# Performance work log

Hardware: AMD Instinct MI355X
Metric: run time of the kernel (lower is better)

Reference implementation:

```python
import jax, jax.numpy as jnp
import numpy as np

B, S, D, H = 4, 2048, 1024, 16
DK = D // H


def setup_inputs() -> dict:
    key = jax.random.key(0)
    ks = jax.random.split(key, 12)
    s = 1.0 / np.sqrt(D)
    inp = {
        "q": jax.random.normal(ks[0], (B, S, D), jnp.float32),
        "k": jax.random.normal(ks[1], (B, S, D), jnp.float32),
        "v": jax.random.normal(ks[2], (B, S, D), jnp.float32),
        # causal mask, broadcastable over batch and heads
        "mask": jnp.tril(jnp.ones((S, S), jnp.int32))[None, None, :, :],
        "Wq": jax.random.uniform(ks[3], (D, D), jnp.float32, -s, s),
        "bq": jax.random.uniform(ks[4], (D,), jnp.float32, -s, s),
        "Wk": jax.random.uniform(ks[5], (D, D), jnp.float32, -s, s),
        "bk": jax.random.uniform(ks[6], (D,), jnp.float32, -s, s),
        "Wv": jax.random.uniform(ks[7], (D, D), jnp.float32, -s, s),
        "bv": jax.random.uniform(ks[8], (D,), jnp.float32, -s, s),
        "Wo": jax.random.uniform(ks[9], (D, D), jnp.float32, -s, s),
        "bo": jax.random.uniform(ks[10], (D,), jnp.float32, -s, s),
    }
    return inp


def reference(q, k, v, mask, Wq, bq, Wk, bk, Wv, bv, Wo, bo):
    def split_heads(x):  # [B,S,D] -> [B,H,S,DK]
        return x.reshape(B, S, H, DK).transpose(0, 2, 1, 3)

    qh = split_heads(q @ Wq.T + bq)
    kh = split_heads(k @ Wk.T + bk)
    vh = split_heads(v @ Wv.T + bv)

    scores = jnp.einsum("bhqd,bhkd->bhqk", qh, kh) / jnp.sqrt(jnp.float32(DK))
    scores = jnp.where(mask == 0, jnp.float32(-1e9), scores)
    attn = jax.nn.softmax(scores, axis=-1)
    out = jnp.einsum("bhqk,bhkd->bhqd", attn, vh)
    out = out.transpose(0, 2, 1, 3).reshape(B, S, D)
    return out @ Wo.T + bo
```

## Files before the change

### kernel.cpp

```cpp
#include <hip/hip_runtime.h>
#include <cstdint>

#define Bb 4
#define Ss 2048
#define Dd 1024
#define Hh 16

typedef unsigned short u16;
typedef unsigned int u32;
typedef __attribute__((ext_vector_type(8))) short short8;
typedef __attribute__((ext_vector_type(8))) _Float16 half8;
typedef __attribute__((ext_vector_type(2))) __fp16 fp16x2;
typedef __attribute__((ext_vector_type(4))) float floatx4;
typedef __attribute__((ext_vector_type(16))) float floatx16;
typedef __attribute__((address_space(3))) u32 lds_u32;
typedef const __attribute__((address_space(1))) u32 glob_u32;

__device__ __forceinline__ u16 f2bf(float x) {
  union { float f; u32 u; } v; v.f = x;
  u32 r = v.u + 0x7fffu + ((v.u >> 16) & 1u);
  return (u16)(r >> 16);
}

__device__ __forceinline__ u32 pk2(float a, float b) {
  union { fp16x2 h; u32 u; } cv;
  cv.h = __builtin_amdgcn_cvt_pkrtz(a, b);
  return cv.u;
}

__device__ __forceinline__ half8 h8_from(u32 a, u32 b, u32 c, u32 d) {
  union { u32 u[4]; half8 h; } t;
  t.u[0] = a; t.u[1] = b; t.u[2] = c; t.u[3] = d;
  return t.h;
}

__global__ __launch_bounds__(256) void cvt_many(const float* __restrict__ s0,
                                                const float* __restrict__ s1,
                                                const float* __restrict__ s2,
                                                const float* __restrict__ s3,
                                                u16* __restrict__ d0,
                                                u16* __restrict__ d1,
                                                u16* __restrict__ d2,
                                                u16* __restrict__ d3, int n8) {
  int z = blockIdx.y;
  const float* s = z == 0 ? s0 : z == 1 ? s1 : z == 2 ? s2 : s3;
  u16* d = z == 0 ? d0 : z == 1 ? d1 : z == 2 ? d2 : d3;
  int i = blockIdx.x * 256 + threadIdx.x;
  if (i >= n8) return;
  const float4* sp = (const float4*)s;
  float4 a = sp[2 * i], b = sp[2 * i + 1];
  u32 w0 = (u32)f2bf(a.x) | ((u32)f2bf(a.y) << 16);
  u32 w1 = (u32)f2bf(a.z) | ((u32)f2bf(a.w) << 16);
  u32 w2 = (u32)f2bf(b.x) | ((u32)f2bf(b.y) << 16);
  u32 w3 = (u32)f2bf(b.z) | ((u32)f2bf(b.w) << 16);
  ((uint4*)d)[i] = make_uint4(w0, w1, w2, w3);
}

template <int MODE>
__device__ __forceinline__ void gemm_body(const u16* __restrict__ A,
                                          const u16* __restrict__ Bw,
                                          const float* __restrict__ bias,
                                          void* __restrict__ Cout, float scale) {
  __shared__ u16 As[128 * 64];
  __shared__ u16 Bs[128 * 64];
  int tid = threadIdx.x;
  int wave = tid >> 6, lane = tid & 63;
  int quad = lane >> 4, l16 = lane & 15;
  int m0 = blockIdx.x * 128, n0 = blockIdx.y * 128;
  int wr = (wave >> 1) * 64, wc = (wave & 1) * 64;
  int s7 = l16 & 7;
  int srow = wave * 8 + (lane >> 3);
  int gcol = (((lane & 7) ^ (lane >> 3)) << 3);

  floatx4 vzero = {0.f, 0.f, 0.f, 0.f};
  floatx4 acc[4][4];
#pragma unroll
  for (int i = 0; i < 4; ++i)
#pragma unroll
    for (int j = 0; j < 4; ++j) acc[i][j] = vzero;

  for (int kt = 0; kt < Dd; kt += 64) {
    __syncthreads();
#pragma unroll
    for (int c = 0; c < 4; ++c) {
      int r = c * 32 + srow;
      __builtin_amdgcn_global_load_lds(
          (glob_u32*)&A[(size_t)(m0 + r) * Dd + kt + gcol],
          (lds_u32*)&As[(c * 32 + wave * 8) * 64], 16, 0, 0);
      __builtin_amdgcn_global_load_lds(
          (glob_u32*)&Bw[(size_t)(n0 + r) * Dd + kt + gcol],
          (lds_u32*)&Bs[(c * 32 + wave * 8) * 64], 16, 0, 0);
    }
    __syncthreads();
#pragma unroll
    for (int kk = 0; kk < 2; ++kk) {
      short8 af[4], bf[4];
#pragma unroll
      for (int i = 0; i < 4; ++i)
        af[i] = *(const short8*)&As[(wr + i * 16 + l16) * 64 + (((quad + 4 * kk) ^ s7) << 3)];
#pragma unroll
      for (int j = 0; j < 4; ++j)
        bf[j] = *(const short8*)&Bs[(wc + j * 16 + l16) * 64 + (((quad + 4 * kk) ^ s7) << 3)];
#pragma unroll
      for (int i = 0; i < 4; ++i)
#pragma unroll
        for (int j = 0; j < 4; ++j)
          acc[i][j] = __builtin_amdgcn_mfma_f32_16x16x32_bf16(af[i], bf[j], acc[i][j], 0, 0, 0);
    }
  }

#pragma unroll
  for (int i = 0; i < 4; ++i) {
#pragma unroll
    for (int j = 0; j < 4; ++j) {
#pragma unroll
      for (int r = 0; r < 4; ++r) {
        int m = m0 + wr + i * 16 + quad * 4 + r;
        int n = n0 + wc + j * 16 + l16;
        float val = (acc[i][j][r] + bias[n]) * scale;
        if (MODE == 0) {
          int b = m >> 11, s = m & (Ss - 1);
          int h = n >> 6, dk = n & 63;
          ((u16*)Cout)[((((size_t)b * Hh + h) * Ss + s) << 6) + dk] = f2bf(val);
        } else {
          ((float*)Cout)[(size_t)m * Dd + n] = val;
        }
      }
    }
  }
}

__global__ __launch_bounds__(256) void gemm_qkv(const u16* qb, const u16* kb, const u16* vb,
                                                const u16* Wq, const u16* Wk, const u16* Wv,
                                                const float* bq, const float* bk, const float* bv,
                                                u16* qo, u16* ko, u16* vo) {
  const float K1 = 0.18033688f;
  int z = blockIdx.z;
  const u16* A = z == 0 ? qb : z == 1 ? kb : vb;
  const u16* W = z == 0 ? Wq : z == 1 ? Wk : Wv;
  const float* bi = z == 0 ? bq : z == 1 ? bk : bv;
  u16* o = z == 0 ? qo : z == 1 ? ko : vo;
  gemm_body<0>(A, W, bi, o, z == 0 ? K1 : 1.0f);
}

__global__ __launch_bounds__(256) void gemm_out(const u16* A, const u16* W,
                                                const float* bi, float* o) {
  gemm_body<1>(A, W, bi, o, 1.0f);
}

__global__ __launch_bounds__(256) void transpose_v(const u16* __restrict__ in,
                                                   _Float16* __restrict__ out) {
  __shared__ u16 T[64 * 72];
  int bh = blockIdx.y, s0 = blockIdx.x * 64, tid = threadIdx.x;
#pragma unroll
  for (int c = 0; c < 2; ++c) {
    int e = c * 2048 + tid * 8;
    int r = e >> 6, col = e & 63;
    *(uint4*)&T[r * 72 + col] = *(const uint4*)&in[((size_t)bh * Ss + s0 + r) * 64 + col];
  }
  __syncthreads();
#pragma unroll
  for (int c = 0; c < 2; ++c) {
    int e = c * 2048 + tid * 8;
    int d = e >> 6, sc = e & 63;
    _Float16 tmp[8];
#pragma unroll
    for (int j = 0; j < 8; ++j) {
      union { u32 u; float f; } cv;
      cv.u = (u32)T[(sc + j) * 72 + d] << 16;
      tmp[j] = (_Float16)cv.f;
    }
    *(uint4*)&out[((size_t)bh * 64 + d) * Ss + s0 + sc] = *(uint4*)tmp;
  }
}

#define MFIX 4.0f
#define SW(a, b) asm("v_permlane32_swap_b32 %0, %1" : "+v"(a), "+v"(b))
#define VRD(CH, NT) \
  (*(const half8*)&Vt[p][((NT) * 32 + l31) * 64 + ((((CH) + hi) ^ s7b) << 3)])

#define TILE_BODY(NST, MASKED)                                                \
  do {                                                                        \
    short8 kf0[4], kf1[4];                                                    \
    _Pragma("unroll") for (int m = 0; m < 4; ++m) {                           \
      kf0[m] = *(const short8*)&Kt[p][l31 * 64 + (((2 * m + hi) ^ s7b) << 3)];\
      if (NST == 2)                                                           \
        kf1[m] = *(const short8*)&Kt[p][(32 + l31) * 64 +                     \
                                        (((2 * m + hi) ^ s7b) << 3)];         \
    }                                                                         \
    floatx16 sc0, sc1;                                                        \
    _Pragma("unroll") for (int r = 0; r < 16; ++r) {                          \
      sc0[r] = -MFIX;                                                         \
      sc1[r] = -MFIX;                                                         \
    }                                                                         \
    __builtin_amdgcn_s_setprio(1);                                            \
    _Pragma("unroll") for (int m = 0; m < 4; ++m) {                           \
      sc0 = __builtin_amdgcn_mfma_f32_32x32x16_bf16(kf0[m], qf[m], sc0, 0, 0, 0); \
      if (NST == 2)                                                           \
        sc1 = __builtin_amdgcn_mfma_f32_32x32x16_bf16(kf1[m], qf[m], sc1, 0, 0, 0); \
    }                                                                         \
    __builtin_amdgcn_s_setprio(0);                                            \
    if (MASKED) {                                                             \
      int qrow = Rq + l31;                                                    \
      _Pragma("unroll") for (int r = 0; r < 16; ++r) {                        \
        int key = k0 + 4 * hi + (r & 3) + 8 * (r >> 2);                       \
        if (key > qrow) sc0[r] = -3e38f;                                      \
        if (NST == 2 && key + 32 > qrow) sc1[r] = -3e38f;                     \
      }                                                                       \
    }                                                                         \
    u32 c0[8], c1[8];                                                         \
    float rs = 0.f;                                                           \
    _Pragma("unroll") for (int j = 0; j < 8; ++j) {                           \
      float p0 = __builtin_amdgcn_exp2f(sc0[2 * j]);                          \
      float p1 = __builtin_amdgcn_exp2f(sc0[2 * j + 1]);                      \
      rs += p0 + p1;                                                          \
      c0[j] = pk2(p0, p1);                                                    \
      if (NST == 2) {                                                         \
        float p2 = __builtin_amdgcn_exp2f(sc1[2 * j]);                        \
        float p3 = __builtin_amdgcn_exp2f(sc1[2 * j + 1]);                    \
        rs += p2 + p3;                                                        \
        c1[j] = pk2(p2, p3);                                                  \
      }                                                                       \
    }                                                                         \
    l_part += rs;                                                             \
    SW(c0[0], c0[2]); SW(c0[1], c0[3]); SW(c0[4], c0[6]); SW(c0[5], c0[7]);   \
    if (NST == 2) {                                                           \
      SW(c1[0], c1[2]); SW(c1[1], c1[3]); SW(c1[4], c1[6]); SW(c1[5], c1[7]); \
    }                                                                         \
    __builtin_amdgcn_s_setprio(1);                                            \
    {                                                                         \
      half8 pa = h8_from(c0[0], c0[1], c0[2], c0[3]);                         \
      o0 = __builtin_amdgcn_mfma_f32_32x32x16_f16(pa, VRD(0, 0), o0, 0, 0, 0);\
      o1 = __builtin_amdgcn_mfma_f32_32x32x16_f16(pa, VRD(0, 1), o1, 0, 0, 0);\
      half8 pb = h8_from(c0[4], c0[5], c0[6], c0[7]);                         \
      o0 = __builtin_amdgcn_mfma_f32_32x32x16_f16(pb, VRD(2, 0), o0, 0, 0, 0);\
      o1 = __builtin_amdgcn_mfma_f32_32x32x16_f16(pb, VRD(2, 1), o1, 0, 0, 0);\
      if (NST == 2) {                                                         \
        half8 pc = h8_from(c1[0], c1[1], c1[2], c1[3]);                       \
        o0 = __builtin_amdgcn_mfma_f32_32x32x16_f16(pc, VRD(4, 0), o0, 0, 0, 0); \
        o1 = __builtin_amdgcn_mfma_f32_32x32x16_f16(pc, VRD(4, 1), o1, 0, 0, 0); \
        half8 pd = h8_from(c1[4], c1[5], c1[6], c1[7]);                       \
        o0 = __builtin_amdgcn_mfma_f32_32x32x16_f16(pd, VRD(6, 0), o0, 0, 0, 0); \
        o1 = __builtin_amdgcn_mfma_f32_32x32x16_f16(pd, VRD(6, 1), o1, 0, 0, 0); \
      }                                                                       \
    }                                                                         \
    __builtin_amdgcn_s_setprio(0);                                            \
  } while (0)

__global__ __launch_bounds__(256) void attn_kernel(const u16* __restrict__ qh,
                                                   const u16* __restrict__ kh,
                                                   const _Float16* __restrict__ vT,
                                                   u16* __restrict__ ctx) {
  __shared__ u16 Kt[2][64 * 64];
  __shared__ _Float16 Vt[2][64 * 64];

  int tid = threadIdx.x, w = tid >> 6, lane = tid & 63;
  int hi = lane >> 5, l31 = lane & 31, s7b = lane & 7;
  int bh = blockIdx.x;
  int sp = blockIdx.y;
  const u16* Q = qh + (size_t)bh * Ss * 64;
  const u16* K = kh + (size_t)bh * Ss * 64;
  const _Float16* V = vT + (size_t)bh * 64 * Ss;

  int Rq = (w < 2) ? 64 * sp + 32 * w : 64 * (31 - sp) + 32 * (w - 2);

  short8 qf[4];
#pragma unroll
  for (int m = 0; m < 4; ++m)
    qf[m] = *(const short8*)&Q[(size_t)(Rq + l31) * 64 + m * 16 + hi * 8];

  floatx16 o0, o1;
#pragma unroll
  for (int r = 0; r < 16; ++r) { o0[r] = 0.f; o1[r] = 0.f; }
  float l_part = 0.f;

  int lrow = w * 8 + (lane >> 3);
  int g8 = ((lane & 7) ^ (lane >> 3)) << 3;
  int nkt = 32 - sp;

#define STAGE(P, KT)                                                          \
  do {                                                                        \
    int _k0 = (KT) * 64;                                                      \
    __builtin_amdgcn_global_load_lds(                                         \
        (glob_u32*)&K[(size_t)(_k0 + lrow) * 64 + g8],                        \
        (lds_u32*)&Kt[P][w * 512], 16, 0, 0);                                 \
    __builtin_amdgcn_global_load_lds(                                         \
        (glob_u32*)&K[(size_t)(_k0 + 32 + lrow) * 64 + g8],                   \
        (lds_u32*)&Kt[P][2048 + w * 512], 16, 0, 0);                          \
    __builtin_amdgcn_global_load_lds(                                         \
        (glob_u32*)&V[(size_t)lrow * Ss + _k0 + g8],                          \
        (lds_u32*)&Vt[P][w * 512], 16, 0, 0);                                 \
    __builtin_amdgcn_global_load_lds(                                         \
        (glob_u32*)&V[(size_t)(32 + lrow) * Ss + _k0 + g8],                   \
        (lds_u32*)&Vt[P][2048 + w * 512], 16, 0, 0);                          \
  } while (0)

  STAGE(0, 0);

  int p = 0;
  for (int kt = 0; kt < nkt; ++kt) {
    int k0 = kt * 64;
    __syncthreads();
    if (kt + 1 < nkt) STAGE(p ^ 1, kt + 1);

    if (k0 + 63 <= Rq) {
      TILE_BODY(2, false);
    } else if (k0 <= Rq + 31) {
      if (k0 + 32 <= Rq + 31) TILE_BODY(2, true);
      else TILE_BODY(1, true);
    }
    p ^= 1;
  }
#undef STAGE

  float l2 = l_part + __shfl_xor(l_part, 32, 64);
  float linv = 1.0f / l2;
  int b = bh >> 4, h = bh & 15;
#pragma unroll
  for (int r = 0; r < 16; ++r) {
    int qi = (r & 3) + 8 * (r >> 2) + 4 * hi;
    float li = __shfl(linv, qi, 64);
    size_t base = ((size_t)b * Ss + Rq + qi) * Dd + h * 64 + l31;
    ctx[base] = f2bf(o0[r] * li);
    ctx[base + 32] = f2bf(o1[r] * li);
  }
}

extern "C" void kernel_launch(void* const* d_in, const int* in_sizes, int n_in,
                              void* d_out, int out_size, void* d_ws, size_t ws_size,
                              hipStream_t stream) {
  const float* q = (const float*)d_in[0];
  const float* k = (const float*)d_in[1];
  const float* v = (const float*)d_in[2];
  const float* Wq = (const float*)d_in[4];
  const float* bq = (const float*)d_in[5];
  const float* Wk = (const float*)d_in[6];
  const float* bk = (const float*)d_in[7];
  const float* Wv = (const float*)d_in[8];
  const float* bv = (const float*)d_in[9];
  const float* Wo = (const float*)d_in[10];
  const float* bo = (const float*)d_in[11];

  char* ws = (char*)d_ws;
  const size_t MB = 1024 * 1024;
  u16* qb = (u16*)(ws + 0 * MB);
  u16* kb = (u16*)(ws + 16 * MB);
  u16* vb = (u16*)(ws + 32 * MB);
  u16* Wqb = (u16*)(ws + 48 * MB);
  u16* Wkb = (u16*)(ws + 50 * MB);
  u16* Wvb = (u16*)(ws + 52 * MB);
  u16* Wob = (u16*)(ws + 54 * MB);
  u16* qhp = (u16*)(ws + 56 * MB);
  u16* khp = (u16*)(ws + 72 * MB);
  u16* vhp = (u16*)(ws + 88 * MB);
  _Float16* vhT = (_Float16*)kb;
  u16* ctx = qb;

  const int nQKV8 = (Bb * Ss * Dd) / 8;
  const int nW8 = (Dd * Dd) / 8;
  {
    dim3 g(nQKV8 / 256, 3);
    cvt_many<<<g, 256, 0, stream>>>(q, k, v, v, qb, kb, vb, vb, nQKV8);
  }
  {
    dim3 g(nW8 / 256, 4);
    cvt_many<<<g, 256, 0, stream>>>(Wq, Wk, Wv, Wo, Wqb, Wkb, Wvb, Wob, nW8);
  }
  {
    dim3 g((Bb * Ss) / 128, Dd / 128, 3);
    gemm_qkv<<<g, 256, 0, stream>>>(qb, kb, vb, Wqb, Wkb, Wvb, bq, bk, bv, qhp, khp, vhp);
  }
  {
    dim3 g(Ss / 64, Bb * Hh);
    transpose_v<<<g, 256, 0, stream>>>(vhp, vhT);
  }
  {
    dim3 g(Bb * Hh, 16);
    attn_kernel<<<g, 256, 0, stream>>>(qhp, khp, vhT, ctx);
  }
  {
    dim3 g((Bb * Ss) / 128, Dd / 128);
    gemm_out<<<g, 256, 0, stream>>>(ctx, Wob, bo, (float*)d_out);
  }
}
```

Measured before the change: 335.3 us.

## Rewrite projection GEMMs as 256x128 double-buffered pipelined kernel with 8 waves

```diff
diff --git a/kernel.cpp b/kernel.cpp
--- a/kernel.cpp
+++ b/kernel.cpp
@@ -56,21 +56,45 @@
   ((uint4*)d)[i] = make_uint4(w0, w1, w2, w3);
 }
 
+#define MFMA_B16 __builtin_amdgcn_mfma_f32_16x16x32_bf16
+
 template <int MODE>
-__device__ __forceinline__ void gemm_body(const u16* __restrict__ A,
-                                          const u16* __restrict__ Bw,
-                                          const float* __restrict__ bias,
-                                          void* __restrict__ Cout, float scale) {
-  __shared__ u16 As[128 * 64];
-  __shared__ u16 Bs[128 * 64];
+__device__ __forceinline__ void gemm256_body(const u16* __restrict__ A,
+                                             const u16* __restrict__ Bw,
+                                             const float* __restrict__ bias,
+                                             void* __restrict__ Cout, float scale) {
+  __shared__ u16 Sa[2][2][128 * 64];
+  __shared__ u16 Sb[2][2][64 * 64];
   int tid = threadIdx.x;
-  int wave = tid >> 6, lane = tid & 63;
+  int w = tid >> 6, lane = tid & 63;
+  int wm = w >> 1, wn = w & 1;
   int quad = lane >> 4, l16 = lane & 15;
-  int m0 = blockIdx.x * 128, n0 = blockIdx.y * 128;
-  int wr = (wave >> 1) * 64, wc = (wave & 1) * 64;
-  int s7 = l16 & 7;
-  int srow = wave * 8 + (lane >> 3);
-  int gcol = (((lane & 7) ^ (lane >> 3)) << 3);
+  int s7 = l16 & 15 & 7;
+  int m0 = blockIdx.x * 256, n0 = blockIdx.y * 128;
+  int srow = tid >> 3;
+  int gcol = (((tid & 7) ^ ((tid >> 3) & 7)) << 3);
+  int ha = wm >> 1;
+  int ra = (wm & 1) * 64;
+
+#define SG_A(BUF, KT)                                                         \
+  do {                                                                        \
+    _Pragma("unroll") for (int h = 0; h < 2; ++h)                             \
+    _Pragma("unroll") for (int j = 0; j < 2; ++j)                             \
+      __builtin_amdgcn_global_load_lds(                                       \
+          (glob_u32*)&A[(size_t)(m0 + h * 128 + j * 64 + srow) * Dd +         \
+                        (KT) * 64 + gcol],                                    \
+          (lds_u32*)&Sa[BUF][h][(j * 64 + w * 8) * 64], 16, 0, 0);            \
+  } while (0)
+#define SG_B(BUF, G, KT)                                                      \
+  __builtin_amdgcn_global_load_lds(                                           \
+      (glob_u32*)&Bw[(size_t)(n0 + (G) * 64 + srow) * Dd + (KT) * 64 + gcol], \
+      (lds_u32*)&Sb[BUF][G][(w * 8) * 64], 16, 0, 0)
+#define LDA(BUF, I, KK)                                                       \
+  (*(const short8*)&Sa[BUF][ha][(ra + (I) * 16 + l16) * 64 +                  \
+                                ((((KK) * 4 + quad) ^ s7) << 3)])
+#define LDB(BUF, G, J, KK)                                                    \
+  (*(const short8*)&Sb[BUF][G][(wn * 32 + (J) * 16 + l16) * 64 +              \
+                               ((((KK) * 4 + quad) ^ s7) << 3)])
 
   floatx4 vzero = {0.f, 0.f, 0.f, 0.f};
   floatx4 acc[4][4];
@@ -79,45 +103,97 @@
 #pragma unroll
     for (int j = 0; j < 4; ++j) acc[i][j] = vzero;
 
-  for (int kt = 0; kt < Dd; kt += 64) {
-    __syncthreads();
-#pragma unroll
-    for (int c = 0; c < 4; ++c) {
-      int r = c * 32 + srow;
-      __builtin_amdgcn_global_load_lds(
-          (glob_u32*)&A[(size_t)(m0 + r) * Dd + kt + gcol],
-          (lds_u32*)&As[(c * 32 + wave * 8) * 64], 16, 0, 0);
-      __builtin_amdgcn_global_load_lds(
-          (glob_u32*)&Bw[(size_t)(n0 + r) * Dd + kt + gcol],
-          (lds_u32*)&Bs[(c * 32 + wave * 8) * 64], 16, 0, 0);
-    }
-    __syncthreads();
-#pragma unroll
-    for (int kk = 0; kk < 2; ++kk) {
-      short8 af[4], bf[4];
-#pragma unroll
-      for (int i = 0; i < 4; ++i)
-        af[i] = *(const short8*)&As[(wr + i * 16 + l16) * 64 + (((quad + 4 * kk) ^ s7) << 3)];
-#pragma unroll
-      for (int j = 0; j < 4; ++j)
-        bf[j] = *(const short8*)&Bs[(wc + j * 16 + l16) * 64 + (((quad + 4 * kk) ^ s7) << 3)];
-#pragma unroll
-      for (int i = 0; i < 4; ++i)
-#pragma unroll
-        for (int j = 0; j < 4; ++j)
-          acc[i][j] = __builtin_amdgcn_mfma_f32_16x16x32_bf16(af[i], bf[j], acc[i][j], 0, 0, 0);
-    }
-  }
+  SG_A(0, 0);
+  SG_B(0, 0, 0);
+  SG_B(0, 1, 0);
+  asm volatile("s_waitcnt vmcnt(0)" ::: "memory");
+  __builtin_amdgcn_s_barrier();
+  __builtin_amdgcn_sched_barrier(0);
+
+  const int nkt = Dd / 64;
+  for (int kt = 0; kt < nkt; ++kt) {
+    int bu = kt & 1, nb = bu ^ 1;
+    int pre = (kt + 1 < nkt);
+    int kn = kt + 1;
+
+    short8 a00 = LDA(bu, 0, 0), a01 = LDA(bu, 0, 1);
+    short8 a10 = LDA(bu, 1, 0), a11 = LDA(bu, 1, 1);
+    short8 b000 = LDB(bu, 0, 0, 0), b001 = LDB(bu, 0, 0, 1);
+    short8 b010 = LDB(bu, 0, 1, 0), b011 = LDB(bu, 0, 1, 1);
+    if (pre) SG_A(nb, kn);
+    __builtin_amdgcn_s_barrier();
+    __builtin_amdgcn_s_setprio(1);
+    acc[0][0] = MFMA_B16(a00, b000, acc[0][0], 0, 0, 0);
+    acc[0][0] = MFMA_B16(a01, b001, acc[0][0], 0, 0, 0);
+    acc[0][1] = MFMA_B16(a00, b010, acc[0][1], 0, 0, 0);
+    acc[0][1] = MFMA_B16(a01, b011, acc[0][1], 0, 0, 0);
+    acc[1][0] = MFMA_B16(a10, b000, acc[1][0], 0, 0, 0);
+    acc[1][0] = MFMA_B16(a11, b001, acc[1][0], 0, 0, 0);
+    acc[1][1] = MFMA_B16(a10, b010, acc[1][1], 0, 0, 0);
+    acc[1][1] = MFMA_B16(a11, b011, acc[1][1], 0, 0, 0);
+    __builtin_amdgcn_s_setprio(0);
+    asm volatile("s_waitcnt vmcnt(4)" ::: "memory");
+    __builtin_amdgcn_s_barrier();
+    __builtin_amdgcn_sched_barrier(0);
+
+    short8 b100 = LDB(bu, 1, 0, 0), b101 = LDB(bu, 1, 0, 1);
+    short8 b110 = LDB(bu, 1, 1, 0), b111 = LDB(bu, 1, 1, 1);
+    if (pre) SG_B(nb, 0, kn);
+    __builtin_amdgcn_s_barrier();
+    __builtin_amdgcn_s_setprio(1);
+    acc[0][2] = MFMA_B16(a00, b100, acc[0][2], 0, 0, 0);
+    acc[0][2] = MFMA_B16(a01, b101, acc[0][2], 0, 0, 0);
+    acc[0][3] = MFMA_B16(a00, b110, acc[0][3], 0, 0, 0);
+    acc[0][3] = MFMA_B16(a01, b111, acc[0][3], 0, 0, 0);
+    acc[1][2] = MFMA_B16(a10, b100, acc[1][2], 0, 0, 0);
+    acc[1][2] = MFMA_B16(a11, b101, acc[1][2], 0, 0, 0);
+    acc[1][3] = MFMA_B16(a10, b110, acc[1][3], 0, 0, 0);
+    acc[1][3] = MFMA_B16(a11, b111, acc[1][3], 0, 0, 0);
+    __builtin_amdgcn_s_setprio(0);
+    __builtin_amdgcn_s_barrier();
+    __builtin_amdgcn_sched_barrier(0);
+
+    short8 a20 = LDA(bu, 2, 0), a21 = LDA(bu, 2, 1);
+    short8 a30 = LDA(bu, 3, 0), a31 = LDA(bu, 3, 1);
+    if (pre) SG_B(nb, 1, kn);
+    __builtin_amdgcn_s_barrier();
+    __builtin_amdgcn_s_setprio(1);
+    acc[2][2] = MFMA_B16(a20, b100, acc[2][2], 0, 0, 0);
+    acc[2][2] = MFMA_B16(a21, b101, acc[2][2], 0, 0, 0);
+    acc[2][3] = MFMA_B16(a20, b110, acc[2][3], 0, 0, 0);
+    acc[2][3] = MFMA_B16(a21, b111, acc[2][3], 0, 0, 0);
+    acc[3][2] = MFMA_B16(a30, b100, acc[3][2], 0, 0, 0);
+    acc[3][2] = MFMA_B16(a31, b101, acc[3][2], 0, 0, 0);
+    acc[3][3] = MFMA_B16(a30, b110, acc[3][3], 0, 0, 0);
+    acc[3][3] = MFMA_B16(a31, b111, acc[3][3], 0, 0, 0);
+    acc[2][0] = MFMA_B16(a20, b000, acc[2][0], 0, 0, 0);
+    acc[2][0] = MFMA_B16(a21, b001, acc[2][0], 0, 0, 0);
+    acc[2][1] = MFMA_B16(a20, b010, acc[2][1], 0, 0, 0);
+    acc[2][1] = MFMA_B16(a21, b011, acc[2][1], 0, 0, 0);
+    acc[3][0] = MFMA_B16(a30, b000, acc[3][0], 0, 0, 0);
+    acc[3][0] = MFMA_B16(a31, b001, acc[3][0], 0, 0, 0);
+    acc[3][1] = MFMA_B16(a30, b010, acc[3][1], 0, 0, 0);
+    acc[3][1] = MFMA_B16(a31, b011, acc[3][1], 0, 0, 0);
+    __builtin_amdgcn_s_setprio(0);
+    asm volatile("s_waitcnt vmcnt(1)" ::: "memory");
+    __builtin_amdgcn_s_barrier();
+    __builtin_amdgcn_sched_barrier(0);
+  }
+#undef SG_A
+#undef SG_B
+#undef LDA
+#undef LDB
 
 #pragma unroll
   for (int i = 0; i < 4; ++i) {
 #pragma unroll
-    for (int j = 0; j < 4; ++j) {
+    for (int jj = 0; jj < 4; ++jj) {
+      int g = jj >> 1, j = jj & 1;
+      int n = n0 + g * 64 + wn * 32 + j * 16 + l16;
 #pragma unroll
       for (int r = 0; r < 4; ++r) {
-        int m = m0 + wr + i * 16 + quad * 4 + r;
-        int n = n0 + wc + j * 16 + l16;
-        float val = (acc[i][j][r] + bias[n]) * scale;
+        int m = m0 + wm * 64 + i * 16 + quad * 4 + r;
+        float val = (acc[i][jj][r] + bias[n]) * scale;
         if (MODE == 0) {
           int b = m >> 11, s = m & (Ss - 1);
           int h = n >> 6, dk = n & 63;
@@ -130,7 +206,7 @@
   }
 }
 
-__global__ __launch_bounds__(256) void gemm_qkv(const u16* qb, const u16* kb, const u16* vb,
+__global__ __launch_bounds__(512) void gemm_qkv(const u16* qb, const u16* kb, const u16* vb,
                                                 const u16* Wq, const u16* Wk, const u16* Wv,
                                                 const float* bq, const float* bk, const float* bv,
                                                 u16* qo, u16* ko, u16* vo) {
@@ -140,12 +216,12 @@
   const u16* W = z == 0 ? Wq : z == 1 ? Wk : Wv;
   const float* bi = z == 0 ? bq : z == 1 ? bk : bv;
   u16* o = z == 0 ? qo : z == 1 ? ko : vo;
-  gemm_body<0>(A, W, bi, o, z == 0 ? K1 : 1.0f);
-}
-
-__global__ __launch_bounds__(256) void gemm_out(const u16* A, const u16* W,
+  gemm256_body<0>(A, W, bi, o, z == 0 ? K1 : 1.0f);
+}
+
+__global__ __launch_bounds__(512) void gemm_out(const u16* A, const u16* W,
                                                 const float* bi, float* o) {
-  gemm_body<1>(A, W, bi, o, 1.0f);
+  gemm256_body<1>(A, W, bi, o, 1.0f);
 }
 
 __global__ __launch_bounds__(256) void transpose_v(const u16* __restrict__ in,
@@ -367,8 +443,8 @@
     cvt_many<<<g, 256, 0, stream>>>(Wq, Wk, Wv, Wo, Wqb, Wkb, Wvb, Wob, nW8);
   }
   {
-    dim3 g((Bb * Ss) / 128, Dd / 128, 3);
-    gemm_qkv<<<g, 256, 0, stream>>>(qb, kb, vb, Wqb, Wkb, Wvb, bq, bk, bv, qhp, khp, vhp);
+    dim3 g((Bb * Ss) / 256, Dd / 128, 3);
+    gemm_qkv<<<g, 512, 0, stream>>>(qb, kb, vb, Wqb, Wkb, Wvb, bq, bk, bv, qhp, khp, vhp);
   }
   {
     dim3 g(Ss / 64, Bb * Hh);
@@ -379,7 +455,7 @@
     attn_kernel<<<g, 256, 0, stream>>>(qhp, khp, vhT, ctx);
   }
   {
-    dim3 g((Bb * Ss) / 128, Dd / 128);
-    gemm_out<<<g, 256, 0, stream>>>(ctx, Wob, bo, (float*)d_out);
-  }
-}
+    dim3 g((Bb * Ss) / 256, Dd / 128);
+    gemm_out<<<g, 512, 0, stream>>>(ctx, Wob, bo, (float*)d_out);
+  }
+}
```

Measured after the change: 342.7 us. 2.2% more time.

## Fuse fp32-to-bf16 input conversion and V transpose into QKV projection GEMM

Applied to the files above, without the earlier changes.

```diff
diff --git a/kernel.cpp b/kernel.cpp
--- a/kernel.cpp
+++ b/kernel.cpp
@@ -20,6 +20,12 @@
   union { float f; u32 u; } v; v.f = x;
   u32 r = v.u + 0x7fffu + ((v.u >> 16) & 1u);
   return (u16)(r >> 16);
+}
+
+__device__ __forceinline__ u32 pkbf(float a, float b) {
+  u32 r;
+  asm("v_cvt_pk_bf16_f32 %0, %1, %2" : "=v"(r) : "v"(a), "v"(b));
+  return r;
 }
 
 __device__ __forceinline__ u32 pk2(float a, float b) {
@@ -57,10 +63,11 @@
 }
 
 template <int MODE>
-__device__ __forceinline__ void gemm_body(const u16* __restrict__ A,
+__device__ __forceinline__ void gemm_body(const void* __restrict__ Av,
                                           const u16* __restrict__ Bw,
                                           const float* __restrict__ bias,
-                                          void* __restrict__ Cout, float scale) {
+                                          void* __restrict__ Cout, float scale,
+                                          int vtrans) {
   __shared__ u16 As[128 * 64];
   __shared__ u16 Bs[128 * 64];
   int tid = threadIdx.x;
@@ -71,6 +78,34 @@
   int s7 = l16 & 7;
   int srow = wave * 8 + (lane >> 3);
   int gcol = (((lane & 7) ^ (lane >> 3)) << 3);
+  int arow = tid >> 3;
+  int ac8 = tid & 7;
+
+  const float* Af = (const float*)Av;
+  const u16* Ab = (const u16*)Av;
+  float4 ar[4][2];
+
+#define LOADA(KT)                                                             \
+  do {                                                                        \
+    _Pragma("unroll") for (int c = 0; c < 4; ++c) {                           \
+      const float4* sp_ = (const float4*)&Af[(size_t)(m0 + c * 32 + arow) *   \
+                                             Dd + (KT) * 64 + ac8 * 8];       \
+      ar[c][0] = sp_[0];                                                      \
+      ar[c][1] = sp_[1];                                                      \
+    }                                                                         \
+  } while (0)
+#define WRITEA()                                                              \
+  do {                                                                        \
+    _Pragma("unroll") for (int c = 0; c < 4; ++c) {                           \
+      int row_ = c * 32 + arow;                                               \
+      union { u32 u[4]; short8 s; } pk_;                                      \
+      pk_.u[0] = pkbf(ar[c][0].x, ar[c][0].y);                                \
+      pk_.u[1] = pkbf(ar[c][0].z, ar[c][0].w);                                \
+      pk_.u[2] = pkbf(ar[c][1].x, ar[c][1].y);                                \
+      pk_.u[3] = pkbf(ar[c][1].z, ar[c][1].w);                                \
+      *(short8*)&As[row_ * 64 + ((ac8 ^ (row_ & 7)) << 3)] = pk_.s;           \
+    }                                                                         \
+  } while (0)
 
   floatx4 vzero = {0.f, 0.f, 0.f, 0.f};
   floatx4 acc[4][4];
@@ -79,19 +114,26 @@
 #pragma unroll
     for (int j = 0; j < 4; ++j) acc[i][j] = vzero;
 
+  if (MODE == 0) LOADA(0);
+
   for (int kt = 0; kt < Dd; kt += 64) {
     __syncthreads();
-#pragma unroll
-    for (int c = 0; c < 4; ++c) {
-      int r = c * 32 + srow;
+    if (MODE == 0) {
+      WRITEA();
+    } else {
+#pragma unroll
+      for (int c = 0; c < 4; ++c)
+        __builtin_amdgcn_global_load_lds(
+            (glob_u32*)&Ab[(size_t)(m0 + c * 32 + srow) * Dd + kt + gcol],
+            (lds_u32*)&As[(c * 32 + wave * 8) * 64], 16, 0, 0);
+    }
+#pragma unroll
+    for (int c = 0; c < 4; ++c)
       __builtin_amdgcn_global_load_lds(
-          (glob_u32*)&A[(size_t)(m0 + r) * Dd + kt + gcol],
-          (lds_u32*)&As[(c * 32 + wave * 8) * 64], 16, 0, 0);
-      __builtin_amdgcn_global_load_lds(
-          (glob_u32*)&Bw[(size_t)(n0 + r) * Dd + kt + gcol],
+          (glob_u32*)&Bw[(size_t)(n0 + c * 32 + srow) * Dd + kt + gcol],
           (lds_u32*)&Bs[(c * 32 + wave * 8) * 64], 16, 0, 0);
-    }
     __syncthreads();
+    if (MODE == 0 && kt + 64 < Dd) LOADA((kt >> 6) + 1);
 #pragma unroll
     for (int kk = 0; kk < 2; ++kk) {
       short8 af[4], bf[4];
@@ -108,70 +150,59 @@
           acc[i][j] = __builtin_amdgcn_mfma_f32_16x16x32_bf16(af[i], bf[j], acc[i][j], 0, 0, 0);
     }
   }
+#undef LOADA
+#undef WRITEA
 
 #pragma unroll
   for (int i = 0; i < 4; ++i) {
 #pragma unroll
     for (int j = 0; j < 4; ++j) {
-#pragma unroll
-      for (int r = 0; r < 4; ++r) {
-        int m = m0 + wr + i * 16 + quad * 4 + r;
-        int n = n0 + wc + j * 16 + l16;
-        float val = (acc[i][j][r] + bias[n]) * scale;
-        if (MODE == 0) {
-          int b = m >> 11, s = m & (Ss - 1);
-          int h = n >> 6, dk = n & 63;
-          ((u16*)Cout)[((((size_t)b * Hh + h) * Ss + s) << 6) + dk] = f2bf(val);
-        } else {
-          ((float*)Cout)[(size_t)m * Dd + n] = val;
+      int n = n0 + wc + j * 16 + l16;
+      if (MODE == 0 && vtrans) {
+        int h = n >> 6, dk = n & 63;
+        int b = m0 >> 11;
+        int sb = (m0 + wr + i * 16 + quad * 4) & (Ss - 1);
+        _Float16 hv[4];
+#pragma unroll
+        for (int r = 0; r < 4; ++r)
+          hv[r] = (_Float16)((acc[i][j][r] + bias[n]) * scale);
+        union { _Float16 h4[4]; uint2 u2; } pv;
+        pv.h4[0] = hv[0]; pv.h4[1] = hv[1]; pv.h4[2] = hv[2]; pv.h4[3] = hv[3];
+        *(uint2*)&((_Float16*)Cout)[((size_t)(b * Hh + h) * 64 + dk) * Ss + sb] = pv.u2;
+      } else {
+#pragma unroll
+        for (int r = 0; r < 4; ++r) {
+          int m = m0 + wr + i * 16 + quad * 4 + r;
+          float val = (acc[i][j][r] + bias[n]) * scale;
+          if (MODE == 0) {
+            int b = m >> 11, s = m & (Ss - 1);
+            int h = n >> 6, dk = n & 63;
+            ((u16*)Cout)[((((size_t)b * Hh + h) * Ss + s) << 6) + dk] = f2bf(val);
+          } else {
+            ((float*)Cout)[(size_t)m * Dd + n] = val;
+          }
         }
       }
     }
   }
 }
 
-__global__ __launch_bounds__(256) void gemm_qkv(const u16* qb, const u16* kb, const u16* vb,
+__global__ __launch_bounds__(256) void gemm_qkv(const float* q, const float* k, const float* v,
                                                 const u16* Wq, const u16* Wk, const u16* Wv,
                                                 const float* bq, const float* bk, const float* bv,
-                                                u16* qo, u16* ko, u16* vo) {
+                                                u16* qo, u16* ko, _Float16* vT) {
   const float K1 = 0.18033688f;
   int z = blockIdx.z;
-  const u16* A = z == 0 ? qb : z == 1 ? kb : vb;
+  const float* A = z == 0 ? q : z == 1 ? k : v;
   const u16* W = z == 0 ? Wq : z == 1 ? Wk : Wv;
   const float* bi = z == 0 ? bq : z == 1 ? bk : bv;
-  u16* o = z == 0 ? qo : z == 1 ? ko : vo;
-  gemm_body<0>(A, W, bi, o, z == 0 ? K1 : 1.0f);
+  void* o = z == 0 ? (void*)qo : z == 1 ? (void*)ko : (void*)vT;
+  gemm_body<0>(A, W, bi, o, z == 0 ? K1 : 1.0f, z == 2);
 }
 
 __global__ __launch_bounds__(256) void gemm_out(const u16* A, const u16* W,
                                                 const float* bi, float* o) {
-  gemm_body<1>(A, W, bi, o, 1.0f);
-}
-
-__global__ __launch_bounds__(256) void transpose_v(const u16* __restrict__ in,
-                                                   _Float16* __restrict__ out) {
-  __shared__ u16 T[64 * 72];
-  int bh = blockIdx.y, s0 = blockIdx.x * 64, tid = threadIdx.x;
-#pragma unroll
-  for (int c = 0; c < 2; ++c) {
-    int e = c * 2048 + tid * 8;
-    int r = e >> 6, col = e & 63;
-    *(uint4*)&T[r * 72 + col] = *(const uint4*)&in[((size_t)bh * Ss + s0 + r) * 64 + col];
-  }
-  __syncthreads();
-#pragma unroll
-  for (int c = 0; c < 2; ++c) {
-    int e = c * 2048 + tid * 8;
-    int d = e >> 6, sc = e & 63;
-    _Float16 tmp[8];
-#pragma unroll
-    for (int j = 0; j < 8; ++j) {
-      union { u32 u; float f; } cv;
-      cv.u = (u32)T[(sc + j) * 72 + d] << 16;
-      tmp[j] = (_Float16)cv.f;
-    }
-    *(uint4*)&out[((size_t)bh * 64 + d) * Ss + s0 + sc] = *(uint4*)tmp;
-  }
+  gemm_body<1>(A, W, bi, o, 1.0f, 0);
 }
 
 #define MFIX 4.0f
@@ -343,36 +374,23 @@
 
   char* ws = (char*)d_ws;
   const size_t MB = 1024 * 1024;
-  u16* qb = (u16*)(ws + 0 * MB);
-  u16* kb = (u16*)(ws + 16 * MB);
-  u16* vb = (u16*)(ws + 32 * MB);
-  u16* Wqb = (u16*)(ws + 48 * MB);
-  u16* Wkb = (u16*)(ws + 50 * MB);
-  u16* Wvb = (u16*)(ws + 52 * MB);
-  u16* Wob = (u16*)(ws + 54 * MB);
-  u16* qhp = (u16*)(ws + 56 * MB);
-  u16* khp = (u16*)(ws + 72 * MB);
-  u16* vhp = (u16*)(ws + 88 * MB);
-  _Float16* vhT = (_Float16*)kb;
-  u16* ctx = qb;
-
-  const int nQKV8 = (Bb * Ss * Dd) / 8;
+  _Float16* vhT = (_Float16*)(ws + 0 * MB);
+  u16* ctx = (u16*)(ws + 16 * MB);
+  u16* Wqb = (u16*)(ws + 32 * MB);
+  u16* Wkb = (u16*)(ws + 34 * MB);
+  u16* Wvb = (u16*)(ws + 36 * MB);
+  u16* Wob = (u16*)(ws + 38 * MB);
+  u16* qhp = (u16*)(ws + 40 * MB);
+  u16* khp = (u16*)(ws + 56 * MB);
+
   const int nW8 = (Dd * Dd) / 8;
-  {
-    dim3 g(nQKV8 / 256, 3);
-    cvt_many<<<g, 256, 0, stream>>>(q, k, v, v, qb, kb, vb, vb, nQKV8);
-  }
   {
     dim3 g(nW8 / 256, 4);
     cvt_many<<<g, 256, 0, stream>>>(Wq, Wk, Wv, Wo, Wqb, Wkb, Wvb, Wob, nW8);
   }
   {
     dim3 g((Bb * Ss) / 128, Dd / 128, 3);
-    gemm_qkv<<<g, 256, 0, stream>>>(qb, kb, vb, Wqb, Wkb, Wvb, bq, bk, bv, qhp, khp, vhp);
-  }
-  {
-    dim3 g(Ss / 64, Bb * Hh);
-    transpose_v<<<g, 256, 0, stream>>>(vhp, vhT);
+    gemm_qkv<<<g, 256, 0, stream>>>(q, k, v, Wqb, Wkb, Wvb, bq, bk, bv, qhp, khp, vhT);
   }
   {
     dim3 g(Bb * Hh, 16);
```

After: 336.8 us. Within noise of the previous version (+0.4%).
